# Performance work log

Measured on AMD Instinct MI355X. Metric: run time of the kernel, lower is better.

The kernel has to match this reference:

```python
import jax, jax.numpy as jnp
import numpy as np

BUCKET_SIZE = 128
CAUSAL = True
LOOK_BACKWARD = 1
LOOK_FORWARD = 0


def look_around(x, backward=LOOK_BACKWARD, forward=LOOK_FORWARD, pad_value=-1.0):
    # x: [n, buckets, bucket_size, ...]; pad along bucket dim, gather halo windows along dim 2
    nb = x.shape[1]
    pad = [(0, 0), (backward, forward)] + [(0, 0)] * (x.ndim - 2)
    p = jnp.pad(x, pad, constant_values=pad_value)
    return jnp.concatenate([p[:, i:i + nb] for i in range(forward + backward + 1)], axis=2)


def setup_inputs() -> dict:
    key = jax.random.key(0)
    kq, kk, kv = jax.random.split(key, 3)
    shape = (4, 16, 8192, 64)  # [batch, heads, seq, head_dim]
    return {
        "q": jax.random.normal(kq, shape, jnp.float32),
        "k": jax.random.normal(kk, shape, jnp.float32),
        "v": jax.random.normal(kv, shape, jnp.float32),
    }


def reference(q, k, v):
    b, h, t, e = q.shape
    buckets = t // BUCKET_SIZE
    ticker = jnp.arange(t, dtype=q.dtype).reshape(1, buckets, BUCKET_SIZE)

    def bkt(x):
        return x.reshape(b * h, buckets, BUCKET_SIZE, e)

    bq, bk, bv = bkt(q), bkt(k), bkt(v)
    bk = look_around(bk)
    bv = look_around(bv)
    bq_t = ticker                # [1, buckets, bucket_size]
    bq_k = look_around(ticker)

    dots = jnp.einsum('nbie,nbje->nbij', bq, bk) * (e ** -0.5)
    mask_value = -jnp.finfo(dots.dtype).max
    if CAUSAL:
        causal_mask = bq_t[:, :, :, None] < bq_k[:, :, None, :]
        dots = jnp.where(causal_mask, mask_value, dots)
    pad_mask = bq_k[:, :, None, :] == -1
    dots = jnp.where(pad_mask, mask_value, dots)

    attn = jax.nn.softmax(dots, axis=-1)
    out = jnp.einsum('nbij,nbje->nbie', attn, bv)
    return out.reshape(b, h, t, e)
```

## Files before the change

kernel.cpp:

```cpp
#include <hip/hip_runtime.h>
#include <hip/hip_bf16.h>

#define T_SEQ 8192
#define E 64
#define BS 128
#define W 256

typedef __attribute__((ext_vector_type(4))) float f32x4;
typedef __attribute__((ext_vector_type(8))) short bf16x8;

__device__ __forceinline__ unsigned short f2bf(float x) {
    union { float f; unsigned u; } v; v.f = x;
    unsigned r = v.u + 0x7fffu + ((v.u >> 16) & 1u);
    return (unsigned short)(r >> 16);
}
__device__ __forceinline__ unsigned pk2(float a, float b) {
    return (unsigned)f2bf(a) | ((unsigned)f2bf(b) << 16);
}

union Frag { unsigned u[4]; bf16x8 v; };

__global__ __launch_bounds__(256, 2)
void la_kernel(const float* __restrict__ q, const float* __restrict__ k,
               const float* __restrict__ v, float* __restrict__ out) {
    __shared__ __align__(16) unsigned char smem[32768];
    unsigned short* KV = (unsigned short*)smem;
    float* OB = (float*)smem;

    const int raw  = blockIdx.x;
    const int work = (raw & 7) * 512 + (raw >> 3);
    const int bh = work >> 6;
    const int qb = work & 63;

    const int tid  = threadIdx.x;
    const int wv   = tid >> 6;
    const int lane = tid & 63;
    const int g    = lane >> 4;
    const int col  = lane & 15;

    const size_t base_kv = (size_t)bh * T_SEQ * E;
    const int k0 = (qb - 1) * BS;

    bf16x8 qf0[2], qf1[2];
    {
        #pragma unroll
        for (int it = 0; it < 2; ++it) {
            #pragma unroll
            for (int kq = 0; kq < 2; ++kq) {
                const float* src = q + ((size_t)bh * T_SEQ + qb * BS + wv * 32 + it * 16 + col) * E
                                     + g * 8 + kq * 32;
                float4 f0 = *(const float4*)(src);
                float4 f1 = *(const float4*)(src + 4);
                Frag fr;
                fr.u[0] = pk2(f0.x, f0.y); fr.u[1] = pk2(f0.z, f0.w);
                fr.u[2] = pk2(f1.x, f1.y); fr.u[3] = pk2(f1.z, f1.w);
                if (it) qf1[kq] = fr.v; else qf0[kq] = fr.v;
            }
        }
    }

    {
        const int jr = tid >> 4;
        const int c4 = (tid & 15) * 4;
        #pragma unroll
        for (int t = 0; t < 16; ++t) {
            const int jj = jr + t * 16;
            const int gk = k0 + jj;
            float4 kvv = make_float4(0.f, 0.f, 0.f, 0.f);
            if (gk >= 0) kvv = *(const float4*)(k + base_kv + (size_t)gk * E + c4);
            uint2 pr;
            pr.x = pk2(kvv.x, kvv.y);
            pr.y = pk2(kvv.z, kvv.w);
            *(uint2*)(&KV[(jj * 64 + c4) ^ ((jj & 7) << 3)]) = pr;
        }
    }
    __syncthreads();

    unsigned P0[32], P1[32];

    auto s_phase = [&](const int it, const bf16x8* qf, unsigned* __restrict__ P) {
        const int NT = 2 * wv + it + 9;
        f32x4 S[16];
        #pragma unroll
        for (int jt = 0; jt < 16; ++jt) S[jt] = (f32x4)0.f;
        #pragma unroll
        for (int jt = 0; jt < 16; ++jt) {
            if (jt < NT) {
                const int j = jt * 16 + col;
                #pragma unroll
                for (int kq = 0; kq < 2; ++kq) {
                    const int e = g * 8 + kq * 32;
                    bf16x8 kf = *(const bf16x8*)(&KV[(j * 64 + e) ^ ((j & 7) << 3)]);
                    S[jt] = __builtin_amdgcn_mfma_f32_16x16x32_bf16(kf, qf[kq], S[jt], 0, 0, 0);
                }
            }
        }
        const int ii = wv * 32 + it * 16 + col;
        float mx = -3.0e38f;
        #pragma unroll
        for (int jt = 0; jt < 16; ++jt) {
            if (jt < NT) {
                #pragma unroll
                for (int r = 0; r < 4; ++r) {
                    const int jl = jt * 16 + g * 4 + r;
                    const bool ok = (jl <= ii + BS) && (qb > 0 || jl >= BS);
                    float s = ok ? S[jt][r] * 0.125f : -1.0e30f;
                    S[jt][r] = s;
                    mx = fmaxf(mx, s);
                }
            }
        }
        mx = fmaxf(mx, __shfl_xor(mx, 16, 64));
        mx = fmaxf(mx, __shfl_xor(mx, 32, 64));
        float sum = 0.f;
        #pragma unroll
        for (int jt = 0; jt < 16; ++jt) {
            if (jt < NT) {
                #pragma unroll
                for (int r = 0; r < 4; ++r) {
                    float p = __expf(S[jt][r] - mx);
                    S[jt][r] = p;
                    sum += p;
                }
            }
        }
        sum += __shfl_xor(sum, 16, 64);
        sum += __shfl_xor(sum, 32, 64);
        const float inv = 1.0f / sum;
        const int NKT = wv + 5;
        #pragma unroll
        for (int kt = 0; kt < 8; ++kt) {
            if (kt < NKT) {
                P[4*kt+0] = pk2(S[2*kt  ][0]*inv, S[2*kt  ][1]*inv);
                P[4*kt+1] = pk2(S[2*kt  ][2]*inv, S[2*kt  ][3]*inv);
                P[4*kt+2] = pk2(S[2*kt+1][0]*inv, S[2*kt+1][1]*inv);
                P[4*kt+3] = pk2(S[2*kt+1][2]*inv, S[2*kt+1][3]*inv);
            } else {
                P[4*kt+0] = 0u; P[4*kt+1] = 0u; P[4*kt+2] = 0u; P[4*kt+3] = 0u;
            }
        }
    };
    s_phase(0, qf0, P0);
    s_phase(1, qf1, P1);
    __syncthreads();

    {
        #pragma unroll
        for (int t = 0; t < 8; ++t) {
            const int d4 = tid & 15;
            const int p  = (tid >> 4) + 16 * t;
            const int gk = k0 + 2 * p;
            float4 a = make_float4(0.f,0.f,0.f,0.f), b = make_float4(0.f,0.f,0.f,0.f);
            if (gk >= 0) {
                a = *(const float4*)(v + base_kv + (size_t)gk * E + 4 * d4);
                b = *(const float4*)(v + base_kv + (size_t)(gk + 1) * E + 4 * d4);
            }
            const int d0 = 4 * d4;
            const int jp = 2 * p;
            *(unsigned*)(&KV[((d0    ) * 256 + jp) ^ (((d0    ) & 7) << 3)]) = pk2(a.x, b.x);
            *(unsigned*)(&KV[((d0 + 1) * 256 + jp) ^ (((d0 + 1) & 7) << 3)]) = pk2(a.y, b.y);
            *(unsigned*)(&KV[((d0 + 2) * 256 + jp) ^ (((d0 + 2) & 7) << 3)]) = pk2(a.z, b.z);
            *(unsigned*)(&KV[((d0 + 3) * 256 + jp) ^ (((d0 + 3) & 7) << 3)]) = pk2(a.w, b.w);
        }
    }
    __syncthreads();

    auto pv_phase = [&](const unsigned* __restrict__ P, f32x4* __restrict__ O) {
        #pragma unroll
        for (int dt = 0; dt < 4; ++dt) O[dt] = (f32x4)0.f;
        const int s0 = ((g & 1) << 5) + col;
        const int s1 = s0 + 16;
        const bool hiSel = (g >= 2);
        const int NKT = wv + 5;
        #pragma unroll
        for (int kt = 0; kt < 8; ++kt) {
            if (kt < NKT) {
                const unsigned x0 = P[4*kt+0], x1 = P[4*kt+1], y0 = P[4*kt+2], y1 = P[4*kt+3];
                unsigned t0x = (unsigned)__shfl((int)x0, s0, 64), t0y = (unsigned)__shfl((int)y0, s0, 64);
                unsigned t1x = (unsigned)__shfl((int)x1, s0, 64), t1y = (unsigned)__shfl((int)y1, s0, 64);
                unsigned t2x = (unsigned)__shfl((int)x0, s1, 64), t2y = (unsigned)__shfl((int)y0, s1, 64);
                unsigned t3x = (unsigned)__shfl((int)x1, s1, 64), t3y = (unsigned)__shfl((int)y1, s1, 64);
                Frag af;
                af.u[0] = hiSel ? t0y : t0x;
                af.u[1] = hiSel ? t1y : t1x;
                af.u[2] = hiSel ? t2y : t2x;
                af.u[3] = hiSel ? t3y : t3x;
                const int j0 = kt * 32 + g * 8;
                #pragma unroll
                for (int dt = 0; dt < 4; ++dt) {
                    const int d = dt * 16 + col;
                    bf16x8 vf = *(const bf16x8*)(&KV[(d * 256 + j0) ^ ((d & 7) << 3)]);
                    O[dt] = __builtin_amdgcn_mfma_f32_16x16x32_bf16(af.v, vf, O[dt], 0, 0, 0);
                }
            }
        }
    };
    f32x4 O0[4], O1[4];
    pv_phase(P0, O0);
    pv_phase(P1, O1);
    __syncthreads();

    #pragma unroll
    for (int it2 = 0; it2 < 2; ++it2) {
        const f32x4* O = it2 ? O1 : O0;
        #pragma unroll
        for (int dt = 0; dt < 4; ++dt) {
            #pragma unroll
            for (int r = 0; r < 4; ++r) {
                const int row = wv * 32 + it2 * 16 + g * 4 + r;
                const int d = dt * 16 + col;
                OB[(row * 64 + d) ^ ((row & 7) << 2)] = O[dt][r];
            }
        }
    }
    __syncthreads();
    {
        #pragma unroll
        for (int t = 0; t < 8; ++t) {
            const int f4  = t * 256 + tid;
            const int row = f4 >> 4;
            const int c4  = (f4 & 15) * 4;
            float4 val = *(const float4*)(&OB[(row * 64 + c4) ^ ((row & 7) << 2)]);
            *(float4*)(out + ((size_t)bh * T_SEQ + qb * BS + row) * E + c4) = val;
        }
    }
}

extern "C" void kernel_launch(void* const* d_in, const int* in_sizes, int n_in,
                              void* d_out, int out_size, void* d_ws, size_t ws_size,
                              hipStream_t stream) {
    const float* q = (const float*)d_in[0];
    const float* k = (const float*)d_in[1];
    const float* v = (const float*)d_in[2];
    float* out = (float*)d_out;
    la_kernel<<<dim3(64 * 64), dim3(256), 0, stream>>>(q, k, v, out);
}
```

Measured before the change: 162.6 us.

## Fold scale into Q, use exp2, defer normalization, skip padded tiles, simplify masks

Folds the softmax scale and log2(e) into Q at load time so softmax can use the hardware exp2 instruction directly. Causal masking is applied only to the diagonal tile instead of every element, and for the first bucket the padded key tiles are skipped in both the QK and PV MMAs. The 1/sum normalization moves from the P values to the final output via lane shuffles, and bf16 conversion uses the library intrinsic. It also rearranges the thread mapping of the V load. Pre-scaling Q in bf16 changes rounding slightly.

After: 157.3 us. -3.3%, faster.

```diff
diff --git a/kernel.cpp b/kernel.cpp
--- a/kernel.cpp
+++ b/kernel.cpp
@@ -4,18 +4,21 @@
 #define T_SEQ 8192
 #define E 64
 #define BS 128
-#define W 256
+#define QSCALE 0.18033688f
 
 typedef __attribute__((ext_vector_type(4))) float f32x4;
 typedef __attribute__((ext_vector_type(8))) short bf16x8;
 
-__device__ __forceinline__ unsigned short f2bf(float x) {
-    union { float f; unsigned u; } v; v.f = x;
-    unsigned r = v.u + 0x7fffu + ((v.u >> 16) & 1u);
-    return (unsigned short)(r >> 16);
-}
+__device__ __forceinline__ float hw_exp2(float x) {
+    float r;
+    asm("v_exp_f32 %0, %1" : "=v"(r) : "v"(x));
+    return r;
+}
+
 __device__ __forceinline__ unsigned pk2(float a, float b) {
-    return (unsigned)f2bf(a) | ((unsigned)f2bf(b) << 16);
+    __hip_bfloat162 h = __float22bfloat162_rn(make_float2(a, b));
+    union { __hip_bfloat162 h; unsigned u; } cv; cv.h = h;
+    return cv.u;
 }
 
 union Frag { unsigned u[4]; bf16x8 v; };
@@ -40,22 +43,24 @@
 
     const size_t base_kv = (size_t)bh * T_SEQ * E;
     const int k0 = (qb - 1) * BS;
+    const int STT = (qb == 0) ? 8 : 0;
+    const int SKT = (qb == 0) ? 4 : 0;
 
     bf16x8 qf0[2], qf1[2];
-    {
-        #pragma unroll
-        for (int it = 0; it < 2; ++it) {
-            #pragma unroll
-            for (int kq = 0; kq < 2; ++kq) {
-                const float* src = q + ((size_t)bh * T_SEQ + qb * BS + wv * 32 + it * 16 + col) * E
-                                     + g * 8 + kq * 32;
-                float4 f0 = *(const float4*)(src);
-                float4 f1 = *(const float4*)(src + 4);
-                Frag fr;
-                fr.u[0] = pk2(f0.x, f0.y); fr.u[1] = pk2(f0.z, f0.w);
-                fr.u[2] = pk2(f1.x, f1.y); fr.u[3] = pk2(f1.z, f1.w);
-                if (it) qf1[kq] = fr.v; else qf0[kq] = fr.v;
-            }
+    #pragma unroll
+    for (int it = 0; it < 2; ++it) {
+        #pragma unroll
+        for (int kq = 0; kq < 2; ++kq) {
+            const float* src = q + ((size_t)bh * T_SEQ + qb * BS + wv * 32 + it * 16 + col) * E
+                                 + g * 8 + kq * 32;
+            float4 f0 = *(const float4*)(src);
+            float4 f1 = *(const float4*)(src + 4);
+            Frag fr;
+            fr.u[0] = pk2(f0.x * QSCALE, f0.y * QSCALE);
+            fr.u[1] = pk2(f0.z * QSCALE, f0.w * QSCALE);
+            fr.u[2] = pk2(f1.x * QSCALE, f1.y * QSCALE);
+            fr.u[3] = pk2(f1.z * QSCALE, f1.w * QSCALE);
+            if (it) qf1[kq] = fr.v; else qf0[kq] = fr.v;
         }
     }
 
@@ -77,15 +82,16 @@
     __syncthreads();
 
     unsigned P0[32], P1[32];
-
-    auto s_phase = [&](const int it, const bf16x8* qf, unsigned* __restrict__ P) {
+    float inv0, inv1;
+
+    auto s_phase = [&](const int it, const bf16x8* qf, unsigned* __restrict__ P, float& inv_out) {
         const int NT = 2 * wv + it + 9;
         f32x4 S[16];
         #pragma unroll
         for (int jt = 0; jt < 16; ++jt) S[jt] = (f32x4)0.f;
         #pragma unroll
         for (int jt = 0; jt < 16; ++jt) {
-            if (jt < NT) {
+            if (jt >= STT && jt < NT) {
                 const int j = jt * 16 + col;
                 #pragma unroll
                 for (int kq = 0; kq < 2; ++kq) {
@@ -95,18 +101,20 @@
                 }
             }
         }
-        const int ii = wv * 32 + it * 16 + col;
         float mx = -3.0e38f;
         #pragma unroll
         for (int jt = 0; jt < 16; ++jt) {
-            if (jt < NT) {
-                #pragma unroll
-                for (int r = 0; r < 4; ++r) {
-                    const int jl = jt * 16 + g * 4 + r;
-                    const bool ok = (jl <= ii + BS) && (qb > 0 || jl >= BS);
-                    float s = ok ? S[jt][r] * 0.125f : -1.0e30f;
-                    S[jt][r] = s;
-                    mx = fmaxf(mx, s);
+            if (jt >= STT && jt < NT) {
+                if (jt == NT - 1) {
+                    #pragma unroll
+                    for (int r = 0; r < 4; ++r) {
+                        float s = (4 * g + r <= col) ? S[jt][r] : -1.0e30f;
+                        S[jt][r] = s;
+                        mx = fmaxf(mx, s);
+                    }
+                } else {
+                    #pragma unroll
+                    for (int r = 0; r < 4; ++r) mx = fmaxf(mx, S[jt][r]);
                 }
             }
         }
@@ -115,10 +123,10 @@
         float sum = 0.f;
         #pragma unroll
         for (int jt = 0; jt < 16; ++jt) {
-            if (jt < NT) {
+            if (jt >= STT && jt < NT) {
                 #pragma unroll
                 for (int r = 0; r < 4; ++r) {
-                    float p = __expf(S[jt][r] - mx);
+                    float p = hw_exp2(S[jt][r] - mx);
                     S[jt][r] = p;
                     sum += p;
                 }
@@ -126,36 +134,36 @@
         }
         sum += __shfl_xor(sum, 16, 64);
         sum += __shfl_xor(sum, 32, 64);
-        const float inv = 1.0f / sum;
+        inv_out = 1.0f / sum;
         const int NKT = wv + 5;
         #pragma unroll
         for (int kt = 0; kt < 8; ++kt) {
-            if (kt < NKT) {
-                P[4*kt+0] = pk2(S[2*kt  ][0]*inv, S[2*kt  ][1]*inv);
-                P[4*kt+1] = pk2(S[2*kt  ][2]*inv, S[2*kt  ][3]*inv);
-                P[4*kt+2] = pk2(S[2*kt+1][0]*inv, S[2*kt+1][1]*inv);
-                P[4*kt+3] = pk2(S[2*kt+1][2]*inv, S[2*kt+1][3]*inv);
+            if (kt >= SKT && kt < NKT) {
+                P[4*kt+0] = pk2(S[2*kt  ][0], S[2*kt  ][1]);
+                P[4*kt+1] = pk2(S[2*kt  ][2], S[2*kt  ][3]);
+                P[4*kt+2] = pk2(S[2*kt+1][0], S[2*kt+1][1]);
+                P[4*kt+3] = pk2(S[2*kt+1][2], S[2*kt+1][3]);
             } else {
                 P[4*kt+0] = 0u; P[4*kt+1] = 0u; P[4*kt+2] = 0u; P[4*kt+3] = 0u;
             }
         }
     };
-    s_phase(0, qf0, P0);
-    s_phase(1, qf1, P1);
+    s_phase(0, qf0, P0, inv0);
+    s_phase(1, qf1, P1, inv1);
     __syncthreads();
 
     {
+        const int d0 = (tid >> 4) * 4;
+        const int pb = tid & 15;
         #pragma unroll
         for (int t = 0; t < 8; ++t) {
-            const int d4 = tid & 15;
-            const int p  = (tid >> 4) + 16 * t;
+            const int p  = pb + 16 * t;
             const int gk = k0 + 2 * p;
             float4 a = make_float4(0.f,0.f,0.f,0.f), b = make_float4(0.f,0.f,0.f,0.f);
             if (gk >= 0) {
-                a = *(const float4*)(v + base_kv + (size_t)gk * E + 4 * d4);
-                b = *(const float4*)(v + base_kv + (size_t)(gk + 1) * E + 4 * d4);
-            }
-            const int d0 = 4 * d4;
+                a = *(const float4*)(v + base_kv + (size_t)gk * E + d0);
+                b = *(const float4*)(v + base_kv + (size_t)(gk + 1) * E + d0);
+            }
             const int jp = 2 * p;
             *(unsigned*)(&KV[((d0    ) * 256 + jp) ^ (((d0    ) & 7) << 3)]) = pk2(a.x, b.x);
             *(unsigned*)(&KV[((d0 + 1) * 256 + jp) ^ (((d0 + 1) & 7) << 3)]) = pk2(a.y, b.y);
@@ -174,7 +182,7 @@
         const int NKT = wv + 5;
         #pragma unroll
         for (int kt = 0; kt < 8; ++kt) {
-            if (kt < NKT) {
+            if (kt >= SKT && kt < NKT) {
                 const unsigned x0 = P[4*kt+0], x1 = P[4*kt+1], y0 = P[4*kt+2], y1 = P[4*kt+3];
                 unsigned t0x = (unsigned)__shfl((int)x0, s0, 64), t0y = (unsigned)__shfl((int)y0, s0, 64);
                 unsigned t1x = (unsigned)__shfl((int)x1, s0, 64), t1y = (unsigned)__shfl((int)y1, s0, 64);
@@ -200,16 +208,25 @@
     pv_phase(P1, O1);
     __syncthreads();
 
+    const int srcbase = (lane & 48) | ((4 * (lane >> 4)) & 15);
+    float w0[4], w1[4];
+    #pragma unroll
+    for (int r = 0; r < 4; ++r) {
+        w0[r] = __shfl(inv0, srcbase + r, 64);
+        w1[r] = __shfl(inv1, srcbase + r, 64);
+    }
+
     #pragma unroll
     for (int it2 = 0; it2 < 2; ++it2) {
         const f32x4* O = it2 ? O1 : O0;
+        const float* w = it2 ? w1 : w0;
         #pragma unroll
         for (int dt = 0; dt < 4; ++dt) {
             #pragma unroll
             for (int r = 0; r < 4; ++r) {
                 const int row = wv * 32 + it2 * 16 + g * 4 + r;
                 const int d = dt * 16 + col;
-                OB[(row * 64 + d) ^ ((row & 7) << 2)] = O[dt][r];
+                OB[(row * 64 + d) ^ ((row & 7) << 2)] = O[dt][r] * w[r];
             }
         }
     }
```
